# Kernel optimization log

Hardware: AMD Instinct MI355X
Metric: run time of the kernel (lower is better)

## Reference

```python
import jax, jax.numpy as jnp
import numpy as np

N_NODES = 100000
N_EDGES = 1600000
IN_DIM, H1, H2, OUT_DIM = 128, 64, 64, 64


def _glorot(key, shape):
    fan_in, fan_out = shape
    lim = np.sqrt(6.0 / (fan_in + fan_out)).astype(np.float32)
    return jax.random.uniform(key, shape, jnp.float32, -lim, lim)


def setup_inputs() -> dict:
    key = jax.random.key(0)
    ks = jax.random.split(key, 8)
    x = jax.random.normal(ks[0], (N_NODES, IN_DIM), jnp.float32)
    edge_index = jax.random.randint(ks[1], (2, N_EDGES), 0, N_NODES, jnp.int64)
    W1 = _glorot(ks[2], (IN_DIM, H1))
    b1 = jnp.zeros((H1,), jnp.float32)
    W2 = _glorot(ks[3], (H1, H2))
    b2 = jnp.zeros((H2,), jnp.float32)
    Wfc = _glorot(ks[4], (H2, OUT_DIM))
    bfc = jnp.zeros((OUT_DIM,), jnp.float32)
    return {"x": x, "W1": W1, "b1": b1, "W2": W2, "b2": b2,
            "Wfc": Wfc, "bfc": bfc, "edge_index": edge_index}


def _gcn_conv(x, src, dst, dinv, W, b, n_nodes):
    # PyG GCNConv: h = D^{-1/2} (A + I) D^{-1/2} (x W) + b
    h = x @ W                                   # [N, out]
    norm = dinv[src] * dinv[dst]                # [E'] edge weights
    msg = norm[:, None] * h[src]                # gather + scale, [E', out]
    agg = jax.ops.segment_sum(msg, dst, num_segments=n_nodes)
    return agg + b


def reference(x, W1, b1, W2, b2, Wfc, bfc, edge_index):
    n = x.shape[0]
    loop = jnp.arange(n, dtype=edge_index.dtype)
    src = jnp.concatenate([edge_index[0], loop])   # self-loops appended
    dst = jnp.concatenate([edge_index[1], loop])
    deg = jnp.zeros((n,), x.dtype).at[dst].add(1.0)  # degree incl. self-loop
    dinv = jax.lax.rsqrt(deg)

    h = jax.nn.relu(_gcn_conv(x, src, dst, dinv, W1, b1, n))
    h = jax.nn.relu(_gcn_conv(h, src, dst, dinv, W2, b2, n))
    embedding = h
    logits = h @ Wfc + bfc
    return embedding, logits
```

## Files before the change

kernel.cpp:

```cpp
#include <hip/hip_runtime.h>
#include <hip/hip_bf16.h>


constexpr int IN_DIM  = 128;
constexpr int HDIM    = 64;
constexpr int NBLK_A  = 256;
constexpr int BSH     = 8;
constexpr int MAXNB   = 512;
constexpr int PADSLK  = 1792;

typedef short bf16x8 __attribute__((ext_vector_type(8)));
typedef float f32x4  __attribute__((ext_vector_type(4)));

__device__ __forceinline__ float bf2f(unsigned int u) {
    return __uint_as_float(u << 16);
}
__device__ __forceinline__ unsigned short f2bf_bits(float f) {
    __hip_bfloat16 b = __float2bfloat16(f);
    return *(unsigned short*)&b;
}


__global__ void binA_count(const int* __restrict__ dst, int* __restrict__ histg,
                           int E, int NB, int chunk) {
    __shared__ int h[MAXNB];
    for (int i = threadIdx.x; i < NB; i += 256) h[i] = 0;
    __syncthreads();
    int beg = blockIdx.x * chunk;
    int end = min(E, beg + chunk);
    for (int e = beg + threadIdx.x; e < end; e += 256)
        atomicAdd(&h[dst[e] >> BSH], 1);
    __syncthreads();
    for (int i = threadIdx.x; i < NB; i += 256)
        histg[i * NBLK_A + blockIdx.x] = h[i];
}

__global__ void binA_scanblocks(int* __restrict__ histg, int* __restrict__ btot) {
    __shared__ int sm[NBLK_A];
    int tid = threadIdx.x;
    int v = histg[blockIdx.x * NBLK_A + tid];
    sm[tid] = v;
    __syncthreads();
    for (int off = 1; off < NBLK_A; off <<= 1) {
        int t = (tid >= off) ? sm[tid - off] : 0;
        __syncthreads();
        sm[tid] += t;
        __syncthreads();
    }
    histg[blockIdx.x * NBLK_A + tid] = sm[tid] - v;
    if (tid == NBLK_A - 1) btot[blockIdx.x] = sm[tid];
}

__device__ __forceinline__ void bucket_scan(const int* __restrict__ btot,
                                            int* bb, int NB) {
    int tid = threadIdx.x;
    for (int i = tid; i < MAXNB; i += 256) bb[i] = (i < NB) ? btot[i] : 0;
    __syncthreads();
    for (int off = 1; off < MAXNB; off <<= 1) {
        int i0 = tid, i1 = tid + 256;
        int t0 = (i0 >= off) ? bb[i0 - off] : 0;
        int t1 = (i1 >= off) ? bb[i1 - off] : 0;
        __syncthreads();
        bb[i0] += t0;
        bb[i1] += t1;
        __syncthreads();
    }
}

__global__ void binA_scatter(const int* __restrict__ src, const int* __restrict__ dst,
                             const int* __restrict__ histg, const int* __restrict__ btot,
                             int* __restrict__ staging, int E, int NB, int chunk) {
    __shared__ int bb[MAXNB];
    __shared__ int cur[MAXNB];
    bucket_scan(btot, bb, NB);
    for (int i = threadIdx.x; i < NB; i += 256)
        cur[i] = (bb[i] - btot[i]) + histg[i * NBLK_A + blockIdx.x];
    __syncthreads();
    int beg = blockIdx.x * chunk;
    int end = min(E, beg + chunk);
    for (int e = beg + threadIdx.x; e < end; e += 256) {
        int s = src[e];
        int d = dst[e];
        int pos = atomicAdd(&cur[d >> BSH], 1);
        staging[pos] = (s << BSH) | (d & 255);
    }
}

__global__ void binB_finalize(const int* __restrict__ staging, const int* __restrict__ btot,
                              int2* __restrict__ rows, int* __restrict__ esrc,
                              float* __restrict__ dinv, unsigned int* __restrict__ hp_rowN,
                              int N, int NB) {
    __shared__ int bb[MAXNB];
    __shared__ int cnt[256], sm[256], cur[256];
    int tid = threadIdx.x;
    int b = blockIdx.x;
    bucket_scan(btot, bb, NB);
    int node0 = b << BSH;
    int nloc = min(256, N - node0);
    int eend = bb[b];
    int ebeg = eend - btot[b];
    int ebegP = ebeg + b * PADSLK;
    cnt[tid] = 0;
    __syncthreads();
    for (int e = ebeg + tid; e < eend; e += 256)
        atomicAdd(&cnt[staging[e] & 255], 1);
    __syncthreads();
    int v = cnt[tid];
    int pv = (v + 7) & ~7;
    sm[tid] = pv;
    __syncthreads();
    for (int off = 1; off < 256; off <<= 1) {
        int t = (tid >= off) ? sm[tid - off] : 0;
        __syncthreads();
        sm[tid] += t;
        __syncthreads();
    }
    int excl = sm[tid] - pv;
    cur[tid] = excl;
    __syncthreads();
    if (tid < nloc) {
        rows[node0 + tid] = make_int2(ebegP + excl, ebegP + excl + pv);
        dinv[node0 + tid] = rsqrtf((float)v + 1.0f);
        for (int q = v; q < pv; ++q)
            esrc[ebegP + excl + q] = N;
    }
    if (b == 0 && tid < 32) hp_rowN[tid] = 0u;
    for (int e = ebeg + tid; e < eend; e += 256) {
        int p = staging[e];
        int pos = ebegP + atomicAdd(&cur[p & 255], 1);
        esrc[pos] = p >> BSH;
    }
}

template<int K, bool IBF16, bool SCALE, bool BIAS, bool OBF16>
__device__ __forceinline__ void mfma_gemm_body(
        const void* __restrict__ Xv, const float* __restrict__ W,
        const float* __restrict__ bias, const float* __restrict__ dinv,
        void* __restrict__ Yv, int n) {
    constexpr int STR = K + 8;
    __shared__ short SMEM[2 * 64 * STR];
    __shared__ float dls[64];
    short* At = SMEM;
    short* Wt = SMEM + 64 * STR;
    const int tid = threadIdx.x;
    const int node0 = blockIdx.x * 64;
    const int w = tid >> 6;
    const int lane = tid & 63;
    const int lrow = lane & 15;
    const int khal = lane >> 4;

    if (IBF16) {
#pragma unroll
        for (int i = 0; i < K / 32; ++i) {
            int s = tid + i * 256;
            int row = s >> 3, j = s & 7;
            int grow = node0 + row;
            uint4 u = make_uint4(0, 0, 0, 0);
            if (grow < n)
                u = *(const uint4*)&((const unsigned short*)Xv)[(size_t)grow * K + j * 8];
            *(uint4*)&At[row * STR + j * 8] = u;
        }
    } else {
#pragma unroll
        for (int i = 0; i < K / 16; ++i) {
            int s = tid + i * 256;
            int row = s / (K / 4), kq = s % (K / 4);
            int grow = node0 + row;
            float4 v = make_float4(0.f, 0.f, 0.f, 0.f);
            if (grow < n)
                v = *(const float4*)&((const float*)Xv)[(size_t)grow * K + kq * 4];
            unsigned short pk[4] = {f2bf_bits(v.x), f2bf_bits(v.y),
                                    f2bf_bits(v.z), f2bf_bits(v.w)};
            *(uint2*)&At[row * STR + kq * 4] = *(uint2*)pk;
        }
    }
#pragma unroll
    for (int i = 0; i < K / 4; ++i) {
        int s = tid + i * 256;
        int k = s >> 6, c = s & 63;
        Wt[c * STR + k] = (short)f2bf_bits(W[s]);
    }
    if (SCALE && tid < 64)
        dls[tid] = (node0 + tid < n) ? dinv[node0 + tid] : 1.0f;
    __syncthreads();

    f32x4 acc[4];
#pragma unroll
    for (int ct = 0; ct < 4; ++ct)
#pragma unroll
        for (int r = 0; r < 4; ++r) acc[ct][r] = 0.f;
#pragma unroll
    for (int kt = 0; kt < K / 32; ++kt) {
        int k0 = kt * 32 + khal * 8;
        bf16x8 a = *(bf16x8*)&At[(w * 16 + lrow) * STR + k0];
#pragma unroll
        for (int ct = 0; ct < 4; ++ct) {
            bf16x8 b = *(bf16x8*)&Wt[(ct * 16 + lrow) * STR + k0];
            acc[ct] = __builtin_amdgcn_mfma_f32_16x16x32_bf16(a, b, acc[ct], 0, 0, 0);
        }
    }
    __syncthreads();

    short* Ot = SMEM;
    float* Of = (float*)SMEM;
#pragma unroll
    for (int ct = 0; ct < 4; ++ct) {
#pragma unroll
        for (int r = 0; r < 4; ++r) {
            int row = w * 16 + khal * 4 + r;
            int col = ct * 16 + lrow;
            float v = acc[ct][r];
            if (BIAS) v += bias[col];
            if (SCALE) v *= dls[row];
            if (OBF16) Ot[row * 72 + col] = (short)f2bf_bits(v);
            else       Of[row * 68 + col] = v;
        }
    }
    __syncthreads();

    if (OBF16) {
#pragma unroll
        for (int i = 0; i < 2; ++i) {
            int s = tid + i * 256;
            int row = s >> 3, j = s & 7;
            if (node0 + row < n)
                *(uint4*)&((unsigned short*)Yv)[(size_t)(node0 + row) * 64 + j * 8] =
                    *(uint4*)&Ot[row * 72 + j * 8];
        }
    } else {
#pragma unroll
        for (int i = 0; i < 4; ++i) {
            int s = tid + i * 256;
            int row = s >> 4, q = s & 15;
            if (node0 + row < n)
                *(float4*)&((float*)Yv)[(size_t)(node0 + row) * 64 + q * 4] =
                    *(float4*)&Of[row * 68 + q * 4];
        }
    }
}

__global__ __launch_bounds__(256, 4) void mgemm1_kernel(
        const float* X, const float* W, const float* dinv, void* Y, int n) {
    mfma_gemm_body<IN_DIM, false, true, false, true>(X, W, nullptr, dinv, Y, n);
}
__global__ __launch_bounds__(256, 4) void mgemm2_kernel(
        const void* X, const float* W, const float* dinv, void* Y, int n) {
    mfma_gemm_body<HDIM, true, true, false, true>(X, W, nullptr, dinv, Y, n);
}
__global__ __launch_bounds__(256, 4) void mfc_kernel(
        const float* X, const float* W, const float* bias, void* Y, int n) {
    mfma_gemm_body<HDIM, false, false, true, false>(X, W, bias, nullptr, Y, n);
}


template<bool OBF16>
__global__ __launch_bounds__(256) void agg_kernel(
        const uint4* __restrict__ hp4, const int* __restrict__ esrc,
        const int2* __restrict__ rows, const float* __restrict__ dinv,
        const float* __restrict__ bias, void* __restrict__ out, int n) {
    const int lane = threadIdx.x & 63;
    const int j = lane & 7;
    const int step = gridDim.x * 32;
    for (int idx = blockIdx.x * 32 + (threadIdx.x >> 6) * 8 + (lane >> 3);
         idx < n; idx += step) {
        const int node = idx;
        const int2 be = rows[node];

        float acc[8];
        {
            uint4 u = hp4[(size_t)node * 8 + j];
            acc[0] = bf2f(u.x & 0xffff); acc[1] = bf2f(u.x >> 16);
            acc[2] = bf2f(u.y & 0xffff); acc[3] = bf2f(u.y >> 16);
            acc[4] = bf2f(u.z & 0xffff); acc[5] = bf2f(u.z >> 16);
            acc[6] = bf2f(u.w & 0xffff); acc[7] = bf2f(u.w >> 16);
        }
        int k = be.x;
        for (; k + 16 <= be.y; k += 16) {
            int s[16];
#pragma unroll
            for (int i = 0; i < 16; ++i)
                s[i] = __builtin_nontemporal_load(&esrc[k + i]);
            uint4 u[16];
#pragma unroll
            for (int i = 0; i < 16; ++i)
                u[i] = hp4[(size_t)s[i] * 8 + j];
#pragma unroll
            for (int i = 0; i < 16; ++i) {
                acc[0] += bf2f(u[i].x & 0xffff); acc[1] += bf2f(u[i].x >> 16);
                acc[2] += bf2f(u[i].y & 0xffff); acc[3] += bf2f(u[i].y >> 16);
                acc[4] += bf2f(u[i].z & 0xffff); acc[5] += bf2f(u[i].z >> 16);
                acc[6] += bf2f(u[i].w & 0xffff); acc[7] += bf2f(u[i].w >> 16);
            }
        }
        if (k < be.y) {
            int s[8];
#pragma unroll
            for (int i = 0; i < 8; ++i)
                s[i] = __builtin_nontemporal_load(&esrc[k + i]);
            uint4 u[8];
#pragma unroll
            for (int i = 0; i < 8; ++i)
                u[i] = hp4[(size_t)s[i] * 8 + j];
#pragma unroll
            for (int i = 0; i < 8; ++i) {
                acc[0] += bf2f(u[i].x & 0xffff); acc[1] += bf2f(u[i].x >> 16);
                acc[2] += bf2f(u[i].y & 0xffff); acc[3] += bf2f(u[i].y >> 16);
                acc[4] += bf2f(u[i].z & 0xffff); acc[5] += bf2f(u[i].z >> 16);
                acc[6] += bf2f(u[i].w & 0xffff); acc[7] += bf2f(u[i].w >> 16);
            }
        }
        const float d = dinv[node];
        float o[8];
#pragma unroll
        for (int t = 0; t < 8; ++t)
            o[t] = fmaxf(fmaf(d, acc[t], bias[8 * j + t]), 0.f);

        if (OBF16) {
            uint4 pk;
            pk.x = (unsigned)f2bf_bits(o[0]) | ((unsigned)f2bf_bits(o[1]) << 16);
            pk.y = (unsigned)f2bf_bits(o[2]) | ((unsigned)f2bf_bits(o[3]) << 16);
            pk.z = (unsigned)f2bf_bits(o[4]) | ((unsigned)f2bf_bits(o[5]) << 16);
            pk.w = (unsigned)f2bf_bits(o[6]) | ((unsigned)f2bf_bits(o[7]) << 16);
            ((uint4*)out)[(size_t)node * 8 + j] = pk;
        } else {
            ((float4*)out)[(size_t)node * 16 + 2 * j]     = make_float4(o[0], o[1], o[2], o[3]);
            ((float4*)out)[(size_t)node * 16 + 2 * j + 1] = make_float4(o[4], o[5], o[6], o[7]);
        }
    }
}

extern "C" void kernel_launch(void* const* d_in, const int* in_sizes, int n_in,
                              void* d_out, int out_size, void* d_ws, size_t ws_size,
                              hipStream_t stream) {
    const float* x   = (const float*)d_in[0];
    const float* W1  = (const float*)d_in[1];
    const float* b1  = (const float*)d_in[2];
    const float* W2  = (const float*)d_in[3];
    const float* b2  = (const float*)d_in[4];
    const float* Wfc = (const float*)d_in[5];
    const float* bfc = (const float*)d_in[6];
    const int*  eidx = (const int*)d_in[7];

    const int N = in_sizes[0] / IN_DIM;
    const int E = in_sizes[7] / 2;
    const int* src = eidx;
    const int* dst = eidx + E;

    const int NB    = (N + 255) >> BSH;
    const int chunk = (E + NBLK_A - 1) / NBLK_A;
    const int EP    = E + NB * PADSLK;

    int* p = (int*)d_ws;
    int2* rows = (int2*)p;           p += (size_t)2 * N + 2;
    float* dinv = (float*)p;         p += (size_t)((N + 3) & ~3);
    int* histg = p;                  p += (size_t)((NB * NBLK_A + 3) & ~3);
    int* btot = p;                   p += 512;
    int* esrc = p;                   p += (size_t)((EP + 3) & ~3);
    unsigned short* hp = (unsigned short*)p;   p += (size_t)(N + 1) * 32;
    unsigned short* h1 = (unsigned short*)p;   p += (size_t)N * 32;
    int* staging = (int*)hp;
    unsigned int* hp_rowN = (unsigned int*)(hp + (size_t)N * 64);

    float* emb    = (float*)d_out;
    float* logits = emb + (size_t)N * HDIM;

    binA_count<<<NBLK_A, 256, 0, stream>>>(dst, histg, E, NB, chunk);
    binA_scanblocks<<<NB, NBLK_A, 0, stream>>>(histg, btot);
    binA_scatter<<<NBLK_A, 256, 0, stream>>>(src, dst, histg, btot, staging, E, NB, chunk);
    binB_finalize<<<NB, 256, 0, stream>>>(staging, btot, rows, esrc, dinv, hp_rowN, N, NB);

    const int mB = (N + 63) / 64;
    const int aBlocks = 2048;

    mgemm1_kernel<<<mB, 256, 0, stream>>>(x, W1, dinv, hp, N);
    agg_kernel<true><<<aBlocks, 256, 0, stream>>>(
        (const uint4*)hp, esrc, rows, dinv, b1, h1, N);

    mgemm2_kernel<<<mB, 256, 0, stream>>>(h1, W2, dinv, hp, N);
    agg_kernel<false><<<aBlocks, 256, 0, stream>>>(
        (const uint4*)hp, esrc, rows, dinv, b2, emb, N);

    mfc_kernel<<<mB, 256, 0, stream>>>(emb, Wfc, bfc, logits, N);
}
```

Before: 286.9 us.

## Fuse CSR build kernels into one persistent kernel with grid barriers

Replaces the four CSR-construction kernels (count, block scan, scatter, finalize) with a single kernel launched with NB blocks that uses atomic-counter grid barriers between phases. The edge chunking is now per-NB-block instead of 256 blocks, and the histogram layout uses a fixed stride of 512. This removes three kernel launch gaps, at the cost of a memset launch, spin-wait barriers, and relying on all NB (~391) blocks being co-resident to avoid deadlock.

Measured after the change: 459.8 us. 1.6x slower.

```diff
diff --git a/kernel.cpp b/kernel.cpp
--- a/kernel.cpp
+++ b/kernel.cpp
@@ -4,9 +4,9 @@
 
 constexpr int IN_DIM  = 128;
 constexpr int HDIM    = 64;
-constexpr int NBLK_A  = 256;
 constexpr int BSH     = 8;
 constexpr int MAXNB   = 512;
+constexpr int HISTW   = 512;
 constexpr int PADSLK  = 1792;
 
 typedef short bf16x8 __attribute__((ext_vector_type(8)));
@@ -21,116 +21,139 @@
 }
 
 
-__global__ void binA_count(const int* __restrict__ dst, int* __restrict__ histg,
-                           int E, int NB, int chunk) {
-    __shared__ int h[MAXNB];
-    for (int i = threadIdx.x; i < NB; i += 256) h[i] = 0;
-    __syncthreads();
-    int beg = blockIdx.x * chunk;
-    int end = min(E, beg + chunk);
-    for (int e = beg + threadIdx.x; e < end; e += 256)
-        atomicAdd(&h[dst[e] >> BSH], 1);
-    __syncthreads();
-    for (int i = threadIdx.x; i < NB; i += 256)
-        histg[i * NBLK_A + blockIdx.x] = h[i];
-}
-
-__global__ void binA_scanblocks(int* __restrict__ histg, int* __restrict__ btot) {
-    __shared__ int sm[NBLK_A];
-    int tid = threadIdx.x;
-    int v = histg[blockIdx.x * NBLK_A + tid];
-    sm[tid] = v;
-    __syncthreads();
-    for (int off = 1; off < NBLK_A; off <<= 1) {
-        int t = (tid >= off) ? sm[tid - off] : 0;
-        __syncthreads();
-        sm[tid] += t;
-        __syncthreads();
-    }
-    histg[blockIdx.x * NBLK_A + tid] = sm[tid] - v;
-    if (tid == NBLK_A - 1) btot[blockIdx.x] = sm[tid];
-}
-
-__device__ __forceinline__ void bucket_scan(const int* __restrict__ btot,
-                                            int* bb, int NB) {
-    int tid = threadIdx.x;
-    for (int i = tid; i < MAXNB; i += 256) bb[i] = (i < NB) ? btot[i] : 0;
-    __syncthreads();
-    for (int off = 1; off < MAXNB; off <<= 1) {
+__device__ __forceinline__ void grid_barrier(int* cnt, int target) {
+    __syncthreads();
+    if (threadIdx.x == 0) {
+        __threadfence();
+        __hip_atomic_fetch_add(cnt, 1, __ATOMIC_ACQ_REL, __HIP_MEMORY_SCOPE_AGENT);
+        while (__hip_atomic_load(cnt, __ATOMIC_ACQUIRE, __HIP_MEMORY_SCOPE_AGENT) < target)
+            __builtin_amdgcn_s_sleep(1);
+    }
+    __syncthreads();
+}
+
+__global__ __launch_bounds__(256) void csr_mega(
+        const int* __restrict__ src, const int* __restrict__ dst,
+        int* __restrict__ histg, int* __restrict__ btot, int* __restrict__ bar,
+        int* __restrict__ staging, int2* __restrict__ rows, int* __restrict__ esrc,
+        float* __restrict__ dinv, unsigned int* __restrict__ hp_rowN,
+        int N, int E, int NB, int chunk) {
+    __shared__ int S0[512];
+    __shared__ int S1[512];
+    __shared__ int S2[256];
+    const int tid = threadIdx.x;
+    const int bid = blockIdx.x;
+
+    for (int i = tid; i < HISTW; i += 256) S0[i] = 0;
+    __syncthreads();
+    {
+        int beg = bid * chunk, end = min(E, beg + chunk);
+        for (int e = beg + tid; e < end; e += 256)
+            atomicAdd(&S0[dst[e] >> BSH], 1);
+    }
+    __syncthreads();
+    for (int i = tid; i < NB; i += 256) histg[(size_t)i * HISTW + bid] = S0[i];
+    grid_barrier(bar, NB);
+
+    {
         int i0 = tid, i1 = tid + 256;
-        int t0 = (i0 >= off) ? bb[i0 - off] : 0;
-        int t1 = (i1 >= off) ? bb[i1 - off] : 0;
-        __syncthreads();
-        bb[i0] += t0;
-        bb[i1] += t1;
-        __syncthreads();
-    }
-}
-
-__global__ void binA_scatter(const int* __restrict__ src, const int* __restrict__ dst,
-                             const int* __restrict__ histg, const int* __restrict__ btot,
-                             int* __restrict__ staging, int E, int NB, int chunk) {
-    __shared__ int bb[MAXNB];
-    __shared__ int cur[MAXNB];
-    bucket_scan(btot, bb, NB);
-    for (int i = threadIdx.x; i < NB; i += 256)
-        cur[i] = (bb[i] - btot[i]) + histg[i * NBLK_A + blockIdx.x];
-    __syncthreads();
-    int beg = blockIdx.x * chunk;
-    int end = min(E, beg + chunk);
-    for (int e = beg + threadIdx.x; e < end; e += 256) {
-        int s = src[e];
-        int d = dst[e];
-        int pos = atomicAdd(&cur[d >> BSH], 1);
-        staging[pos] = (s << BSH) | (d & 255);
-    }
-}
-
-__global__ void binB_finalize(const int* __restrict__ staging, const int* __restrict__ btot,
-                              int2* __restrict__ rows, int* __restrict__ esrc,
-                              float* __restrict__ dinv, unsigned int* __restrict__ hp_rowN,
-                              int N, int NB) {
-    __shared__ int bb[MAXNB];
-    __shared__ int cnt[256], sm[256], cur[256];
-    int tid = threadIdx.x;
-    int b = blockIdx.x;
-    bucket_scan(btot, bb, NB);
-    int node0 = b << BSH;
-    int nloc = min(256, N - node0);
-    int eend = bb[b];
-    int ebeg = eend - btot[b];
-    int ebegP = ebeg + b * PADSLK;
-    cnt[tid] = 0;
-    __syncthreads();
-    for (int e = ebeg + tid; e < eend; e += 256)
-        atomicAdd(&cnt[staging[e] & 255], 1);
-    __syncthreads();
-    int v = cnt[tid];
-    int pv = (v + 7) & ~7;
-    sm[tid] = pv;
-    __syncthreads();
-    for (int off = 1; off < 256; off <<= 1) {
-        int t = (tid >= off) ? sm[tid - off] : 0;
-        __syncthreads();
-        sm[tid] += t;
-        __syncthreads();
-    }
-    int excl = sm[tid] - pv;
-    cur[tid] = excl;
-    __syncthreads();
-    if (tid < nloc) {
-        rows[node0 + tid] = make_int2(ebegP + excl, ebegP + excl + pv);
-        dinv[node0 + tid] = rsqrtf((float)v + 1.0f);
-        for (int q = v; q < pv; ++q)
-            esrc[ebegP + excl + q] = N;
-    }
-    if (b == 0 && tid < 32) hp_rowN[tid] = 0u;
-    for (int e = ebeg + tid; e < eend; e += 256) {
-        int p = staging[e];
-        int pos = ebegP + atomicAdd(&cur[p & 255], 1);
-        esrc[pos] = p >> BSH;
-    }
-}
+        int v0 = (i0 < NB) ? histg[(size_t)bid * HISTW + i0] : 0;
+        int v1 = (i1 < NB) ? histg[(size_t)bid * HISTW + i1] : 0;
+        S0[i0] = v0; S0[i1] = v1;
+        __syncthreads();
+        for (int off = 1; off < 512; off <<= 1) {
+            int t0 = (i0 >= off) ? S0[i0 - off] : 0;
+            int t1 = (i1 >= off) ? S0[i1 - off] : 0;
+            __syncthreads();
+            S0[i0] += t0; S0[i1] += t1;
+            __syncthreads();
+        }
+        if (i0 < NB) histg[(size_t)bid * HISTW + i0] = S0[i0] - v0;
+        if (i1 < NB) histg[(size_t)bid * HISTW + i1] = S0[i1] - v1;
+        if (tid == 255) btot[bid] = S0[511];
+    }
+    grid_barrier(bar, 2 * NB);
+
+    {
+        int i0 = tid, i1 = tid + 256;
+        int b0 = (i0 < NB) ? btot[i0] : 0;
+        int b1 = (i1 < NB) ? btot[i1] : 0;
+        S0[i0] = b0; S0[i1] = b1;
+        __syncthreads();
+        for (int off = 1; off < 512; off <<= 1) {
+            int t0 = (i0 >= off) ? S0[i0 - off] : 0;
+            int t1 = (i1 >= off) ? S0[i1 - off] : 0;
+            __syncthreads();
+            S0[i0] += t0; S0[i1] += t1;
+            __syncthreads();
+        }
+        if (i0 < NB) S1[i0] = (S0[i0] - b0) + histg[(size_t)i0 * HISTW + bid];
+        if (i1 < NB) S1[i1] = (S0[i1] - b1) + histg[(size_t)i1 * HISTW + bid];
+        __syncthreads();
+        int beg = bid * chunk, end = min(E, beg + chunk);
+        for (int e = beg + tid; e < end; e += 256) {
+            int s = src[e];
+            int d = dst[e];
+            int pos = atomicAdd(&S1[d >> BSH], 1);
+            staging[pos] = (s << BSH) | (d & 255);
+        }
+    }
+    grid_barrier(bar, 3 * NB);
+
+    {
+        int i0 = tid, i1 = tid + 256;
+        int b0 = (i0 < NB) ? btot[i0] : 0;
+        int b1 = (i1 < NB) ? btot[i1] : 0;
+        S0[i0] = b0; S0[i1] = b1;
+        __syncthreads();
+        for (int off = 1; off < 512; off <<= 1) {
+            int t0 = (i0 >= off) ? S0[i0 - off] : 0;
+            int t1 = (i1 >= off) ? S0[i1 - off] : 0;
+            __syncthreads();
+            S0[i0] += t0; S0[i1] += t1;
+            __syncthreads();
+        }
+        int eend = S0[bid];
+        int ebeg = eend - btot[bid];
+        int ebegP = ebeg + bid * PADSLK;
+        int node0 = bid << BSH;
+        int nloc = min(256, N - node0);
+        int* cnt = S1;
+        int* sm  = S1 + 256;
+        int* cur = S2;
+        cnt[tid] = 0;
+        __syncthreads();
+        for (int e = ebeg + tid; e < eend; e += 256)
+            atomicAdd(&cnt[staging[e] & 255], 1);
+        __syncthreads();
+        int v = cnt[tid];
+        int pv = (v + 7) & ~7;
+        sm[tid] = pv;
+        __syncthreads();
+        for (int off = 1; off < 256; off <<= 1) {
+            int t = (tid >= off) ? sm[tid - off] : 0;
+            __syncthreads();
+            sm[tid] += t;
+            __syncthreads();
+        }
+        int excl = sm[tid] - pv;
+        cur[tid] = excl;
+        __syncthreads();
+        if (tid < nloc) {
+            rows[node0 + tid] = make_int2(ebegP + excl, ebegP + excl + pv);
+            dinv[node0 + tid] = rsqrtf((float)v + 1.0f);
+            for (int q = v; q < pv; ++q)
+                esrc[ebegP + excl + q] = N;
+        }
+        if (bid == 0 && tid < 32) hp_rowN[tid] = 0u;
+        for (int e = ebeg + tid; e < eend; e += 256) {
+            int p = staging[e];
+            int pos = ebegP + atomicAdd(&cur[p & 255], 1);
+            esrc[pos] = p >> BSH;
+        }
+    }
+}
+
 
 template<int K, bool IBF16, bool SCALE, bool BIAS, bool OBF16>
 __device__ __forceinline__ void mfma_gemm_body(
@@ -347,14 +370,15 @@
     const int* dst = eidx + E;
 
     const int NB    = (N + 255) >> BSH;
-    const int chunk = (E + NBLK_A - 1) / NBLK_A;
+    const int chunk = (E + NB - 1) / NB;
     const int EP    = E + NB * PADSLK;
 
     int* p = (int*)d_ws;
     int2* rows = (int2*)p;           p += (size_t)2 * N + 2;
     float* dinv = (float*)p;         p += (size_t)((N + 3) & ~3);
-    int* histg = p;                  p += (size_t)((NB * NBLK_A + 3) & ~3);
+    int* histg = p;                  p += (size_t)NB * HISTW;
     int* btot = p;                   p += 512;
+    int* bar = p;                    p += 16;
     int* esrc = p;                   p += (size_t)((EP + 3) & ~3);
     unsigned short* hp = (unsigned short*)p;   p += (size_t)(N + 1) * 32;
     unsigned short* h1 = (unsigned short*)p;   p += (size_t)N * 32;
@@ -364,13 +388,12 @@
     float* emb    = (float*)d_out;
     float* logits = emb + (size_t)N * HDIM;
 
-    binA_count<<<NBLK_A, 256, 0, stream>>>(dst, histg, E, NB, chunk);
-    binA_scanblocks<<<NB, NBLK_A, 0, stream>>>(histg, btot);
-    binA_scatter<<<NBLK_A, 256, 0, stream>>>(src, dst, histg, btot, staging, E, NB, chunk);
-    binB_finalize<<<NB, 256, 0, stream>>>(staging, btot, rows, esrc, dinv, hp_rowN, N, NB);
-
     const int mB = (N + 63) / 64;
     const int aBlocks = 2048;
+
+    hipMemsetAsync(bar, 0, 16 * sizeof(int), stream);
+    csr_mega<<<NB, 256, 0, stream>>>(src, dst, histg, btot, bar, staging,
+                                     rows, esrc, dinv, hp_rowN, N, E, NB, chunk);
 
     mgemm1_kernel<<<mB, 256, 0, stream>>>(x, W1, dinv, hp, N);
     agg_kernel<true><<<aBlocks, 256, 0, stream>>>(
```

## Fuse layer-1 GEMM with edge histogram and defer dinv scaling to finalize

Applied to the files above, without the earlier changes.

The first GEMM no longer depends on dinv. It is merged into one launch with the binning count pass, with extra blocks doing the histogram, so both run concurrently. The dinv row scaling of the layer-1 features moves into binB_finalize, which rescales the bf16 rows in place. GEMM tiles grow from 64 to 128 rows per block to reuse W fragments across two row tiles. Staging gets its own workspace buffer instead of aliasing hp. The cost is an extra read-modify-write pass over hp, a second bf16 rounding, and lower occupancy from the larger shared memory.

After: 292.6 us. 1.02x slower.

```diff
diff --git a/kernel.cpp b/kernel.cpp
--- a/kernel.cpp
+++ b/kernel.cpp
@@ -21,18 +21,20 @@
 }
 
 
-__global__ void binA_count(const int* __restrict__ dst, int* __restrict__ histg,
-                           int E, int NB, int chunk) {
-    __shared__ int h[MAXNB];
-    for (int i = threadIdx.x; i < NB; i += 256) h[i] = 0;
-    __syncthreads();
-    int beg = blockIdx.x * chunk;
-    int end = min(E, beg + chunk);
-    for (int e = beg + threadIdx.x; e < end; e += 256)
-        atomicAdd(&h[dst[e] >> BSH], 1);
-    __syncthreads();
-    for (int i = threadIdx.x; i < NB; i += 256)
-        histg[i * NBLK_A + blockIdx.x] = h[i];
+__device__ __forceinline__ void bucket_scan(const int* __restrict__ btot,
+                                            int* bb, int NB) {
+    int tid = threadIdx.x;
+    for (int i = tid; i < MAXNB; i += 256) bb[i] = (i < NB) ? btot[i] : 0;
+    __syncthreads();
+    for (int off = 1; off < MAXNB; off <<= 1) {
+        int i0 = tid, i1 = tid + 256;
+        int t0 = (i0 >= off) ? bb[i0 - off] : 0;
+        int t1 = (i1 >= off) ? bb[i1 - off] : 0;
+        __syncthreads();
+        bb[i0] += t0;
+        bb[i1] += t1;
+        __syncthreads();
+    }
 }
 
 __global__ void binA_scanblocks(int* __restrict__ histg, int* __restrict__ btot) {
@@ -49,22 +51,6 @@
     }
     histg[blockIdx.x * NBLK_A + tid] = sm[tid] - v;
     if (tid == NBLK_A - 1) btot[blockIdx.x] = sm[tid];
-}
-
-__device__ __forceinline__ void bucket_scan(const int* __restrict__ btot,
-                                            int* bb, int NB) {
-    int tid = threadIdx.x;
-    for (int i = tid; i < MAXNB; i += 256) bb[i] = (i < NB) ? btot[i] : 0;
-    __syncthreads();
-    for (int off = 1; off < MAXNB; off <<= 1) {
-        int i0 = tid, i1 = tid + 256;
-        int t0 = (i0 >= off) ? bb[i0 - off] : 0;
-        int t1 = (i1 >= off) ? bb[i1 - off] : 0;
-        __syncthreads();
-        bb[i0] += t0;
-        bb[i1] += t1;
-        __syncthreads();
-    }
 }
 
 __global__ void binA_scatter(const int* __restrict__ src, const int* __restrict__ dst,
@@ -88,10 +74,11 @@
 
 __global__ void binB_finalize(const int* __restrict__ staging, const int* __restrict__ btot,
                               int2* __restrict__ rows, int* __restrict__ esrc,
-                              float* __restrict__ dinv, unsigned int* __restrict__ hp_rowN,
+                              float* __restrict__ dinv, uint4* __restrict__ hp4,
                               int N, int NB) {
     __shared__ int bb[MAXNB];
     __shared__ int cnt[256], sm[256], cur[256];
+    __shared__ float dls[256];
     int tid = threadIdx.x;
     int b = blockIdx.x;
     bucket_scan(btot, bb, NB);
@@ -101,6 +88,7 @@
     int ebeg = eend - btot[b];
     int ebegP = ebeg + b * PADSLK;
     cnt[tid] = 0;
+    dls[tid] = 1.0f;
     __syncthreads();
     for (int e = ebeg + tid; e < eend; e += 256)
         atomicAdd(&cnt[staging[e] & 255], 1);
@@ -119,31 +107,55 @@
     cur[tid] = excl;
     __syncthreads();
     if (tid < nloc) {
+        float d = rsqrtf((float)v + 1.0f);
         rows[node0 + tid] = make_int2(ebegP + excl, ebegP + excl + pv);
-        dinv[node0 + tid] = rsqrtf((float)v + 1.0f);
+        dinv[node0 + tid] = d;
+        dls[tid] = d;
         for (int q = v; q < pv; ++q)
             esrc[ebegP + excl + q] = N;
     }
-    if (b == 0 && tid < 32) hp_rowN[tid] = 0u;
+    if (b == 0 && tid < 8) hp4[(size_t)N * 8 + tid] = make_uint4(0, 0, 0, 0);
     for (int e = ebeg + tid; e < eend; e += 256) {
         int p = staging[e];
         int pos = ebegP + atomicAdd(&cur[p & 255], 1);
         esrc[pos] = p >> BSH;
     }
+    __syncthreads();
+    int m = nloc * 8;
+    uint4* hpq = hp4 + (size_t)node0 * 8;
+    for (int q = tid; q < m; q += 256) {
+        float dd = dls[q >> 3];
+        uint4 u = hpq[q];
+        unsigned int r[4];
+        const unsigned int* up = &u.x;
+#pragma unroll
+        for (int c = 0; c < 4; ++c) {
+            float lo = bf2f(up[c] & 0xffff) * dd;
+            float hi = bf2f(up[c] >> 16) * dd;
+            r[c] = (unsigned)f2bf_bits(lo) | ((unsigned)f2bf_bits(hi) << 16);
+        }
+        hpq[q] = make_uint4(r[0], r[1], r[2], r[3]);
+    }
+}
+
+template<int K, bool OBF16>
+constexpr int smem_bytes() {
+    int stg = (128 + 64) * (K + 8) * 2;
+    int out = OBF16 ? 128 * 72 * 2 : 128 * 68 * 4;
+    return stg > out ? stg : out;
 }
 
 template<int K, bool IBF16, bool SCALE, bool BIAS, bool OBF16>
 __device__ __forceinline__ void mfma_gemm_body(
-        const void* __restrict__ Xv, const float* __restrict__ W,
-        const float* __restrict__ bias, const float* __restrict__ dinv,
-        void* __restrict__ Yv, int n) {
+        char* __restrict__ SMEMC, const void* __restrict__ Xv,
+        const float* __restrict__ W, const float* __restrict__ bias,
+        const float* __restrict__ dinv, void* __restrict__ Yv, int n, int bid) {
     constexpr int STR = K + 8;
-    __shared__ short SMEM[2 * 64 * STR];
-    __shared__ float dls[64];
-    short* At = SMEM;
-    short* Wt = SMEM + 64 * STR;
+    __shared__ float dls[128];
+    short* At = (short*)SMEMC;
+    short* Wt = At + 128 * STR;
     const int tid = threadIdx.x;
-    const int node0 = blockIdx.x * 64;
+    const int node0 = bid * 128;
     const int w = tid >> 6;
     const int lane = tid & 63;
     const int lrow = lane & 15;
@@ -151,9 +163,9 @@
 
     if (IBF16) {
 #pragma unroll
-        for (int i = 0; i < K / 32; ++i) {
+        for (int i = 0; i < K / 16; ++i) {
             int s = tid + i * 256;
-            int row = s >> 3, j = s & 7;
+            int row = s / (K / 8), j = s % (K / 8);
             int grow = node0 + row;
             uint4 u = make_uint4(0, 0, 0, 0);
             if (grow < n)
@@ -162,7 +174,7 @@
         }
     } else {
 #pragma unroll
-        for (int i = 0; i < K / 16; ++i) {
+        for (int i = 0; i < K / 8; ++i) {
             int s = tid + i * 256;
             int row = s / (K / 4), kq = s % (K / 4);
             int grow = node0 + row;
@@ -180,47 +192,57 @@
         int k = s >> 6, c = s & 63;
         Wt[c * STR + k] = (short)f2bf_bits(W[s]);
     }
-    if (SCALE && tid < 64)
+    if (SCALE && tid < 128)
         dls[tid] = (node0 + tid < n) ? dinv[node0 + tid] : 1.0f;
     __syncthreads();
 
-    f32x4 acc[4];
-#pragma unroll
-    for (int ct = 0; ct < 4; ++ct)
-#pragma unroll
-        for (int r = 0; r < 4; ++r) acc[ct][r] = 0.f;
+    f32x4 acc[2][4];
+#pragma unroll
+    for (int rt = 0; rt < 2; ++rt)
+#pragma unroll
+        for (int ct = 0; ct < 4; ++ct)
+#pragma unroll
+            for (int r = 0; r < 4; ++r) acc[rt][ct][r] = 0.f;
 #pragma unroll
     for (int kt = 0; kt < K / 32; ++kt) {
         int k0 = kt * 32 + khal * 8;
-        bf16x8 a = *(bf16x8*)&At[(w * 16 + lrow) * STR + k0];
+        bf16x8 b[4];
+#pragma unroll
+        for (int ct = 0; ct < 4; ++ct)
+            b[ct] = *(bf16x8*)&Wt[(ct * 16 + lrow) * STR + k0];
+#pragma unroll
+        for (int rt = 0; rt < 2; ++rt) {
+            bf16x8 a = *(bf16x8*)&At[(w * 32 + rt * 16 + lrow) * STR + k0];
+#pragma unroll
+            for (int ct = 0; ct < 4; ++ct)
+                acc[rt][ct] = __builtin_amdgcn_mfma_f32_16x16x32_bf16(a, b[ct], acc[rt][ct], 0, 0, 0);
+        }
+    }
+    __syncthreads();
+
+    short* Ot = (short*)SMEMC;
+    float* Of = (float*)SMEMC;
+#pragma unroll
+    for (int rt = 0; rt < 2; ++rt) {
 #pragma unroll
         for (int ct = 0; ct < 4; ++ct) {
-            bf16x8 b = *(bf16x8*)&Wt[(ct * 16 + lrow) * STR + k0];
-            acc[ct] = __builtin_amdgcn_mfma_f32_16x16x32_bf16(a, b, acc[ct], 0, 0, 0);
-        }
-    }
-    __syncthreads();
-
-    short* Ot = SMEM;
-    float* Of = (float*)SMEM;
-#pragma unroll
-    for (int ct = 0; ct < 4; ++ct) {
-#pragma unroll
-        for (int r = 0; r < 4; ++r) {
-            int row = w * 16 + khal * 4 + r;
-            int col = ct * 16 + lrow;
-            float v = acc[ct][r];
-            if (BIAS) v += bias[col];
-            if (SCALE) v *= dls[row];
-            if (OBF16) Ot[row * 72 + col] = (short)f2bf_bits(v);
-            else       Of[row * 68 + col] = v;
+#pragma unroll
+            for (int r = 0; r < 4; ++r) {
+                int row = w * 32 + rt * 16 + khal * 4 + r;
+                int col = ct * 16 + lrow;
+                float v = acc[rt][ct][r];
+                if (BIAS) v += bias[col];
+                if (SCALE) v *= dls[row];
+                if (OBF16) Ot[row * 72 + col] = (short)f2bf_bits(v);
+                else       Of[row * 68 + col] = v;
+            }
         }
     }
     __syncthreads();
 
     if (OBF16) {
 #pragma unroll
-        for (int i = 0; i < 2; ++i) {
+        for (int i = 0; i < 4; ++i) {
             int s = tid + i * 256;
             int row = s >> 3, j = s & 7;
             if (node0 + row < n)
@@ -229,7 +251,7 @@
         }
     } else {
 #pragma unroll
-        for (int i = 0; i < 4; ++i) {
+        for (int i = 0; i < 8; ++i) {
             int s = tid + i * 256;
             int row = s >> 4, q = s & 15;
             if (node0 + row < n)
@@ -239,17 +261,37 @@
     }
 }
 
-__global__ __launch_bounds__(256, 4) void mgemm1_kernel(
-        const float* X, const float* W, const float* dinv, void* Y, int n) {
-    mfma_gemm_body<IN_DIM, false, true, false, true>(X, W, nullptr, dinv, Y, n);
-}
+__global__ __launch_bounds__(256, 2) void gemm1_count_kernel(
+        const float* __restrict__ X, const float* __restrict__ W,
+        unsigned short* __restrict__ Y, const int* __restrict__ dst,
+        int* __restrict__ histg, int E, int NB, int chunk, int n) {
+    __shared__ char SMEMC[smem_bytes<IN_DIM, true>()];
+    if ((int)blockIdx.x < NBLK_A) {
+        int* h = (int*)SMEMC;
+        for (int i = threadIdx.x; i < NB; i += 256) h[i] = 0;
+        __syncthreads();
+        int beg = blockIdx.x * chunk;
+        int end = min(E, beg + chunk);
+        for (int e = beg + threadIdx.x; e < end; e += 256)
+            atomicAdd(&h[dst[e] >> BSH], 1);
+        __syncthreads();
+        for (int i = threadIdx.x; i < NB; i += 256)
+            histg[i * NBLK_A + blockIdx.x] = h[i];
+        return;
+    }
+    mfma_gemm_body<IN_DIM, false, false, false, true>(
+        SMEMC, X, W, nullptr, nullptr, Y, n, (int)blockIdx.x - NBLK_A);
+}
+
 __global__ __launch_bounds__(256, 4) void mgemm2_kernel(
         const void* X, const float* W, const float* dinv, void* Y, int n) {
-    mfma_gemm_body<HDIM, true, true, false, true>(X, W, nullptr, dinv, Y, n);
+    __shared__ char SMEMC[smem_bytes<HDIM, true>()];
+    mfma_gemm_body<HDIM, true, true, false, true>(SMEMC, X, W, nullptr, dinv, Y, n, blockIdx.x);
 }
 __global__ __launch_bounds__(256, 4) void mfc_kernel(
         const float* X, const float* W, const float* bias, void* Y, int n) {
-    mfma_gemm_body<HDIM, false, false, true, false>(X, W, bias, nullptr, Y, n);
+    __shared__ char SMEMC[smem_bytes<HDIM, false>()];
+    mfma_gemm_body<HDIM, false, false, true, false>(SMEMC, X, W, bias, nullptr, Y, n, blockIdx.x);
 }
 
 
@@ -355,24 +397,25 @@
     float* dinv = (float*)p;         p += (size_t)((N + 3) & ~3);
     int* histg = p;                  p += (size_t)((NB * NBLK_A + 3) & ~3);
     int* btot = p;                   p += 512;
+    int* staging = p;                p += (size_t)((E + 3) & ~3);
     int* esrc = p;                   p += (size_t)((EP + 3) & ~3);
     unsigned short* hp = (unsigned short*)p;   p += (size_t)(N + 1) * 32;
     unsigned short* h1 = (unsigned short*)p;   p += (size_t)N * 32;
-    int* staging = (int*)hp;
-    unsigned int* hp_rowN = (unsigned int*)(hp + (size_t)N * 64);
 
     float* emb    = (float*)d_out;
     float* logits = emb + (size_t)N * HDIM;
 
-    binA_count<<<NBLK_A, 256, 0, stream>>>(dst, histg, E, NB, chunk);
+    const int mB = (N + 127) / 128;
+    const int aBlocks = 2048;
+
+    gemm1_count_kernel<<<NBLK_A + mB, 256, 0, stream>>>(
+        x, W1, hp, dst, histg, E, NB, chunk, N);
+
     binA_scanblocks<<<NB, NBLK_A, 0, stream>>>(histg, btot);
     binA_scatter<<<NBLK_A, 256, 0, stream>>>(src, dst, histg, btot, staging, E, NB, chunk);
-    binB_finalize<<<NB, 256, 0, stream>>>(staging, btot, rows, esrc, dinv, hp_rowN, N, NB);
-
-    const int mB = (N + 63) / 64;
-    const int aBlocks = 2048;
-
-    mgemm1_kernel<<<mB, 256, 0, stream>>>(x, W1, dinv, hp, N);
+    binB_finalize<<<NB, 256, 0, stream>>>(staging, btot, rows, esrc, dinv,
+                                          (uint4*)hp, N, NB);
+
     agg_kernel<true><<<aBlocks, 256, 0, stream>>>(
         (const uint4*)hp, esrc, rows, dinv, b1, h1, N);
 
```

## Split bf16 feature table into four column-slab planes for aggregation locality

Applied to the files above, without the earlier changes.

Stores the intermediate bf16 feature tables as four separate planes of 16 columns each, every plane holding N+1 rows, instead of one row-major 64-column table. Groups of aggregation blocks each handle one plane, so the random gather working set per block group shrinks to a quarter and can stay in cache. The cost is that each gathered row segment is 32 bytes instead of 128, so each edge is read four times across the blocks. Staging gets its own workspace region so it no longer aliases the feature buffer, and the GEMMs read and write the planar layout.

Measured after the change: 335.4 us. 1.17x slower.

```diff
diff --git a/kernel.cpp b/kernel.cpp
--- a/kernel.cpp
+++ b/kernel.cpp
@@ -88,8 +88,8 @@
 
 __global__ void binB_finalize(const int* __restrict__ staging, const int* __restrict__ btot,
                               int2* __restrict__ rows, int* __restrict__ esrc,
-                              float* __restrict__ dinv, unsigned int* __restrict__ hp_rowN,
-                              int N, int NB) {
+                              float* __restrict__ dinv, uint2* __restrict__ hpq,
+                              int N, int NB, int NP1) {
     __shared__ int bb[MAXNB];
     __shared__ int cnt[256], sm[256], cur[256];
     int tid = threadIdx.x;
@@ -124,7 +124,8 @@
         for (int q = v; q < pv; ++q)
             esrc[ebegP + excl + q] = N;
     }
-    if (b == 0 && tid < 32) hp_rowN[tid] = 0u;
+    if (b == 0 && tid < 16)
+        hpq[((size_t)(tid >> 2) * NP1 + N) * 4 + (tid & 3)] = make_uint2(0u, 0u);
     for (int e = ebeg + tid; e < eend; e += 256) {
         int p = staging[e];
         int pos = ebegP + atomicAdd(&cur[p & 255], 1);
@@ -136,7 +137,7 @@
 __device__ __forceinline__ void mfma_gemm_body(
         const void* __restrict__ Xv, const float* __restrict__ W,
         const float* __restrict__ bias, const float* __restrict__ dinv,
-        void* __restrict__ Yv, int n) {
+        void* __restrict__ Yv, int n, int NP1) {
     constexpr int STR = K + 8;
     __shared__ short SMEM[2 * 64 * STR];
     __shared__ float dls[64];
@@ -157,7 +158,7 @@
             int grow = node0 + row;
             uint4 u = make_uint4(0, 0, 0, 0);
             if (grow < n)
-                u = *(const uint4*)&((const unsigned short*)Xv)[(size_t)grow * K + j * 8];
+                u = ((const uint4*)Xv)[((size_t)(j >> 1) * NP1 + grow) * 2 + (j & 1)];
             *(uint4*)&At[row * STR + j * 8] = u;
         }
     } else {
@@ -224,7 +225,7 @@
             int s = tid + i * 256;
             int row = s >> 3, j = s & 7;
             if (node0 + row < n)
-                *(uint4*)&((unsigned short*)Yv)[(size_t)(node0 + row) * 64 + j * 8] =
+                ((uint4*)Yv)[((size_t)(j >> 1) * NP1 + node0 + row) * 2 + (j & 1)] =
                     *(uint4*)&Ot[row * 72 + j * 8];
         }
     } else {
@@ -240,56 +241,54 @@
 }
 
 __global__ __launch_bounds__(256, 4) void mgemm1_kernel(
-        const float* X, const float* W, const float* dinv, void* Y, int n) {
-    mfma_gemm_body<IN_DIM, false, true, false, true>(X, W, nullptr, dinv, Y, n);
+        const float* X, const float* W, const float* dinv, void* Y, int n, int NP1) {
+    mfma_gemm_body<IN_DIM, false, true, false, true>(X, W, nullptr, dinv, Y, n, NP1);
 }
 __global__ __launch_bounds__(256, 4) void mgemm2_kernel(
-        const void* X, const float* W, const float* dinv, void* Y, int n) {
-    mfma_gemm_body<HDIM, true, true, false, true>(X, W, nullptr, dinv, Y, n);
+        const void* X, const float* W, const float* dinv, void* Y, int n, int NP1) {
+    mfma_gemm_body<HDIM, true, true, false, true>(X, W, nullptr, dinv, Y, n, NP1);
 }
 __global__ __launch_bounds__(256, 4) void mfc_kernel(
         const float* X, const float* W, const float* bias, void* Y, int n) {
-    mfma_gemm_body<HDIM, false, false, true, false>(X, W, bias, nullptr, Y, n);
-}
-
+    mfma_gemm_body<HDIM, false, false, true, false>(X, W, bias, nullptr, Y, n, 0);
+}
 
 template<bool OBF16>
 __global__ __launch_bounds__(256) void agg_kernel(
-        const uint4* __restrict__ hp4, const int* __restrict__ esrc,
+        const uint2* __restrict__ hpq, const int* __restrict__ esrc,
         const int2* __restrict__ rows, const float* __restrict__ dinv,
-        const float* __restrict__ bias, void* __restrict__ out, int n) {
+        const float* __restrict__ bias, void* __restrict__ out, int n, int NP1) {
     const int lane = threadIdx.x & 63;
-    const int j = lane & 7;
-    const int step = gridDim.x * 32;
-    for (int idx = blockIdx.x * 32 + (threadIdx.x >> 6) * 8 + (lane >> 3);
+    const int j = lane & 3;
+    const int q = ((int)blockIdx.x & 7) >> 1;
+    const uint2* hq = hpq + (size_t)q * NP1 * 4;
+    const int pb = ((int)blockIdx.x >> 3) * 2 + ((int)blockIdx.x & 1);
+    const int step = (gridDim.x >> 2) * 64;
+    const float b0 = bias[q * 16 + 4 * j + 0];
+    const float b1 = bias[q * 16 + 4 * j + 1];
+    const float b2 = bias[q * 16 + 4 * j + 2];
+    const float b3 = bias[q * 16 + 4 * j + 3];
+
+    for (int idx = pb * 64 + (threadIdx.x >> 6) * 16 + (lane >> 2);
          idx < n; idx += step) {
-        const int node = idx;
-        const int2 be = rows[node];
-
-        float acc[8];
-        {
-            uint4 u = hp4[(size_t)node * 8 + j];
-            acc[0] = bf2f(u.x & 0xffff); acc[1] = bf2f(u.x >> 16);
-            acc[2] = bf2f(u.y & 0xffff); acc[3] = bf2f(u.y >> 16);
-            acc[4] = bf2f(u.z & 0xffff); acc[5] = bf2f(u.z >> 16);
-            acc[6] = bf2f(u.w & 0xffff); acc[7] = bf2f(u.w >> 16);
-        }
+        const int2 be = rows[idx];
+        uint2 su = hq[(size_t)idx * 4 + j];
+        float a0 = bf2f(su.x & 0xffff), a1 = bf2f(su.x >> 16);
+        float a2 = bf2f(su.y & 0xffff), a3 = bf2f(su.y >> 16);
         int k = be.x;
         for (; k + 16 <= be.y; k += 16) {
             int s[16];
 #pragma unroll
             for (int i = 0; i < 16; ++i)
                 s[i] = __builtin_nontemporal_load(&esrc[k + i]);
-            uint4 u[16];
+            uint2 u[16];
 #pragma unroll
             for (int i = 0; i < 16; ++i)
-                u[i] = hp4[(size_t)s[i] * 8 + j];
+                u[i] = hq[(size_t)s[i] * 4 + j];
 #pragma unroll
             for (int i = 0; i < 16; ++i) {
-                acc[0] += bf2f(u[i].x & 0xffff); acc[1] += bf2f(u[i].x >> 16);
-                acc[2] += bf2f(u[i].y & 0xffff); acc[3] += bf2f(u[i].y >> 16);
-                acc[4] += bf2f(u[i].z & 0xffff); acc[5] += bf2f(u[i].z >> 16);
-                acc[6] += bf2f(u[i].w & 0xffff); acc[7] += bf2f(u[i].w >> 16);
+                a0 += bf2f(u[i].x & 0xffff); a1 += bf2f(u[i].x >> 16);
+                a2 += bf2f(u[i].y & 0xffff); a3 += bf2f(u[i].y >> 16);
             }
         }
         if (k < be.y) {
@@ -297,34 +296,29 @@
 #pragma unroll
             for (int i = 0; i < 8; ++i)
                 s[i] = __builtin_nontemporal_load(&esrc[k + i]);
-            uint4 u[8];
+            uint2 u[8];
 #pragma unroll
             for (int i = 0; i < 8; ++i)
-                u[i] = hp4[(size_t)s[i] * 8 + j];
+                u[i] = hq[(size_t)s[i] * 4 + j];
 #pragma unroll
             for (int i = 0; i < 8; ++i) {
-                acc[0] += bf2f(u[i].x & 0xffff); acc[1] += bf2f(u[i].x >> 16);
-                acc[2] += bf2f(u[i].y & 0xffff); acc[3] += bf2f(u[i].y >> 16);
-                acc[4] += bf2f(u[i].z & 0xffff); acc[5] += bf2f(u[i].z >> 16);
-                acc[6] += bf2f(u[i].w & 0xffff); acc[7] += bf2f(u[i].w >> 16);
+                a0 += bf2f(u[i].x & 0xffff); a1 += bf2f(u[i].x >> 16);
+                a2 += bf2f(u[i].y & 0xffff); a3 += bf2f(u[i].y >> 16);
             }
         }
-        const float d = dinv[node];
-        float o[8];
-#pragma unroll
-        for (int t = 0; t < 8; ++t)
-            o[t] = fmaxf(fmaf(d, acc[t], bias[8 * j + t]), 0.f);
+        const float d = dinv[idx];
+        float o0 = fmaxf(fmaf(d, a0, b0), 0.f);
+        float o1 = fmaxf(fmaf(d, a1, b1), 0.f);
+        float o2 = fmaxf(fmaf(d, a2, b2), 0.f);
+        float o3 = fmaxf(fmaf(d, a3, b3), 0.f);
 
         if (OBF16) {
-            uint4 pk;
-            pk.x = (unsigned)f2bf_bits(o[0]) | ((unsigned)f2bf_bits(o[1]) << 16);
-            pk.y = (unsigned)f2bf_bits(o[2]) | ((unsigned)f2bf_bits(o[3]) << 16);
-            pk.z = (unsigned)f2bf_bits(o[4]) | ((unsigned)f2bf_bits(o[5]) << 16);
-            pk.w = (unsigned)f2bf_bits(o[6]) | ((unsigned)f2bf_bits(o[7]) << 16);
-            ((uint4*)out)[(size_t)node * 8 + j] = pk;
+            uint2 pk;
+            pk.x = (unsigned)f2bf_bits(o0) | ((unsigned)f2bf_bits(o1) << 16);
+            pk.y = (unsigned)f2bf_bits(o2) | ((unsigned)f2bf_bits(o3) << 16);
+            ((uint2*)out)[((size_t)q * NP1 + idx) * 4 + j] = pk;
         } else {
-            ((float4*)out)[(size_t)node * 16 + 2 * j]     = make_float4(o[0], o[1], o[2], o[3]);
-            ((float4*)out)[(size_t)node * 16 + 2 * j + 1] = make_float4(o[4], o[5], o[6], o[7]);
+            ((float4*)out)[(size_t)idx * 16 + q * 4 + j] = make_float4(o0, o1, o2, o3);
         }
     }
 }
@@ -349,36 +343,37 @@
     const int NB    = (N + 255) >> BSH;
     const int chunk = (E + NBLK_A - 1) / NBLK_A;
     const int EP    = E + NB * PADSLK;
+    const int NP1   = N + 1;
 
     int* p = (int*)d_ws;
     int2* rows = (int2*)p;           p += (size_t)2 * N + 2;
     float* dinv = (float*)p;         p += (size_t)((N + 3) & ~3);
     int* histg = p;                  p += (size_t)((NB * NBLK_A + 3) & ~3);
     int* btot = p;                   p += 512;
+    int* staging = p;                p += (size_t)((E + 3) & ~3);
     int* esrc = p;                   p += (size_t)((EP + 3) & ~3);
-    unsigned short* hp = (unsigned short*)p;   p += (size_t)(N + 1) * 32;
-    unsigned short* h1 = (unsigned short*)p;   p += (size_t)N * 32;
-    int* staging = (int*)hp;
-    unsigned int* hp_rowN = (unsigned int*)(hp + (size_t)N * 64);
+    unsigned short* hp = (unsigned short*)p;   p += (size_t)4 * NP1 * 8;
+    unsigned short* h1 = (unsigned short*)p;   p += (size_t)4 * NP1 * 8;
 
     float* emb    = (float*)d_out;
     float* logits = emb + (size_t)N * HDIM;
+
+    const int mB = (N + 63) / 64;
+    const int aBlocks = 2048;
 
     binA_count<<<NBLK_A, 256, 0, stream>>>(dst, histg, E, NB, chunk);
     binA_scanblocks<<<NB, NBLK_A, 0, stream>>>(histg, btot);
     binA_scatter<<<NBLK_A, 256, 0, stream>>>(src, dst, histg, btot, staging, E, NB, chunk);
-    binB_finalize<<<NB, 256, 0, stream>>>(staging, btot, rows, esrc, dinv, hp_rowN, N, NB);
-
-    const int mB = (N + 63) / 64;
-    const int aBlocks = 2048;
-
-    mgemm1_kernel<<<mB, 256, 0, stream>>>(x, W1, dinv, hp, N);
+    binB_finalize<<<NB, 256, 0, stream>>>(staging, btot, rows, esrc, dinv,
+                                          (uint2*)hp, N, NB, NP1);
+
+    mgemm1_kernel<<<mB, 256, 0, stream>>>(x, W1, dinv, hp, N, NP1);
     agg_kernel<true><<<aBlocks, 256, 0, stream>>>(
-        (const uint4*)hp, esrc, rows, dinv, b1, h1, N);
-
-    mgemm2_kernel<<<mB, 256, 0, stream>>>(h1, W2, dinv, hp, N);
+        (const uint2*)hp, esrc, rows, dinv, b1, h1, N, NP1);
+
+    mgemm2_kernel<<<mB, 256, 0, stream>>>(h1, W2, dinv, hp, N, NP1);
     agg_kernel<false><<<aBlocks, 256, 0, stream>>>(
-        (const uint4*)hp, esrc, rows, dinv, b2, emb, N);
+        (const uint2*)hp, esrc, rows, dinv, b2, emb, N, NP1);
 
     mfc_kernel<<<mB, 256, 0, stream>>>(emb, Wfc, bfc, logits, N);
 }
```
